# Optimization experiments

Measured on AMD Instinct MI355X. Metric: run time of the kernel, lower is better.

Reference implementation:

```python
import jax, jax.numpy as jnp
import numpy as np

H = 16      # q heads
G = 4       # groups (n_rep)
THETA = 10000.0


def _rope(x, cos, sin):
    # x pairs adjacent elements (torch complex view of reshape(..., -1, 2))
    x0 = x[..., ::2]
    x1 = x[..., 1::2]
    r0 = x0 * cos - x1 * sin
    r1 = x0 * sin + x1 * cos
    return jnp.stack([r0, r1], axis=-1).reshape(x.shape)


def setup_inputs() -> dict:
    key = jax.random.key(0)
    ks = jax.random.split(key, 5)
    B, S, D = 2, 2048, 1024
    return {
        "x": jax.random.normal(ks[0], (B, S, D), jnp.float32),
        "Wq": jax.random.normal(ks[1], (D, D), jnp.float32) * 0.02,
        "Wk": jax.random.normal(ks[2], (D, D // G), jnp.float32) * 0.02,
        "Wv": jax.random.normal(ks[3], (D, D // G), jnp.float32) * 0.02,
        "Wo": jax.random.normal(ks[4], (D, D), jnp.float32) * 0.02,
    }


def reference(x, Wq, Wk, Wv, Wo):
    B, S, D = x.shape
    hd = D // H                     # head dim = 64
    Hkv = H // G                    # kv heads = 4

    q = x @ Wq                      # (B,S,D)
    k = x @ Wk                      # (B,S,D/G)
    v = x @ Wv                      # (B,S,D/G)

    # repeat_kv: (B,S,Hkv,hd) -> (B,S,H,hd)
    k = jnp.repeat(k.reshape(B, S, Hkv, hd), G, axis=2)
    v = jnp.repeat(v.reshape(B, S, Hkv, hd), G, axis=2)

    # RoPE angles: freqs precomputed over hidden_dim (as in source)
    inv = 1.0 / (THETA ** (jnp.arange(0, D, 2, dtype=jnp.float32) / D))  # (D/2,)
    ang = jnp.arange(S, dtype=jnp.float32)[:, None] * inv[None, :]       # (S,D/2)
    q = _rope(q, jnp.cos(ang)[None], jnp.sin(ang)[None])                 # (B,S,D)
    angk = ang[:, : hd // 2]                                             # (S,hd/2)
    k = _rope(k, jnp.cos(angk)[None, :, None, :], jnp.sin(angk)[None, :, None, :])

    q = q.reshape(B, S, H, hd).transpose(0, 2, 1, 3)   # (B,H,S,hd)
    k = k.transpose(0, 2, 1, 3)
    v = v.transpose(0, 2, 1, 3)

    # NOTE: scale uses sqrt(hidden_dim), faithful to source
    scores = jnp.einsum('bhqd,bhkd->bhqk', q, k) / jnp.sqrt(jnp.float32(D))
    p = jax.nn.softmax(scores, axis=-1)
    o = jnp.einsum('bhqk,bhkd->bhqd', p, v)
    o = o.transpose(0, 2, 1, 3).reshape(B, S, D)
    return o @ Wo
```

## Files before the change

### kernel.cpp

```cpp
#include <hip/hip_runtime.h>
#include <math.h>

#define BATCH 2
#define SEQ   2048
#define DMODEL 1024
#define KDIM  1024
#define NH    16
#define HDIM  64
#define GRP   4
#define NKV   4
#define NSPLIT 4

enum { M_PLAIN = 0, M_QKV = 1 };

#define LN_THETA 9.210340371976184f

typedef short bf8_t __attribute__((ext_vector_type(8)));
typedef float f4_t __attribute__((ext_vector_type(4)));
typedef unsigned short us4_t __attribute__((ext_vector_type(4)));
typedef unsigned short us8_t __attribute__((ext_vector_type(8)));
typedef _Float16 h_t;
typedef _Float16 h4_t __attribute__((ext_vector_type(4)));

#define QB_OFF 0
#define KB_OFF 4194304
#define VB_OFF (4194304 + 1048576)

__device__ __forceinline__ unsigned short f2bf(float f) {
  unsigned int u = __float_as_uint(f);
  u += 0x7fffu + ((u >> 16) & 1u);
  return (unsigned short)(u >> 16);
}

__device__ __forceinline__ void gload_lds16(const void* g, void* l) {
  typedef __attribute__((address_space(1))) unsigned int gu32;
  typedef __attribute__((address_space(3))) unsigned int lu32;
  __builtin_amdgcn_global_load_lds((const gu32*)g, (lu32*)l, 16, 0, 0);
}

__global__ __launch_bounds__(256) void conv_x(const float* __restrict__ in,
                                              unsigned short* __restrict__ out) {
  const int i = blockIdx.x * 256 + threadIdx.x;
  float4 v = ((const float4*)in)[i];
  us4_t o = {f2bf(v.x), f2bf(v.y), f2bf(v.z), f2bf(v.w)};
  ((us4_t*)out)[i] = o;
}

__global__ __launch_bounds__(256) void convT_all(const float* __restrict__ W0,
                                                 const float* __restrict__ W1,
                                                 const float* __restrict__ W2,
                                                 const float* __restrict__ W3,
                                                 unsigned short* __restrict__ Wqkvt,
                                                 unsigned short* __restrict__ Wot) {
  const float* W; unsigned short* out; int N, rowoff;
  switch (blockIdx.z) {
    case 0: W = W0; out = Wqkvt; N = 1024; rowoff = 0;    break;
    case 1: W = W1; out = Wqkvt; N = 256;  rowoff = 1024; break;
    case 2: W = W2; out = Wqkvt; N = 256;  rowoff = 1280; break;
    default: W = W3; out = Wot;  N = 1024; rowoff = 0;    break;
  }
  const int n0 = blockIdx.x * 64;
  if (n0 >= N) return;
  __shared__ unsigned short T[64][72];
  const int t = threadIdx.x;
  const int k0 = blockIdx.y * 64;
  const int kr = t >> 4, n4 = (t & 15) * 4;
#pragma unroll
  for (int i = 0; i < 4; ++i) {
    const int k = kr + i * 16;
    float4 v = *(const float4*)&W[(size_t)(k0 + k) * N + n0 + n4];
    T[n4 + 0][k] = f2bf(v.x);
    T[n4 + 1][k] = f2bf(v.y);
    T[n4 + 2][k] = f2bf(v.z);
    T[n4 + 3][k] = f2bf(v.w);
  }
  __syncthreads();
#pragma unroll
  for (int i = 0; i < 2; ++i) {
    const int c = t + i * 256;
    const int n = c >> 3, kc = (c & 7) * 8;
    us8_t v = *(const us8_t*)&T[n][kc];
    *(us8_t*)&out[(size_t)(rowoff + n0 + n) * KDIM + k0 + kc] = v;
  }
}

template <int MODE>
__global__ __launch_bounds__(256, 3) void gemm_bf16(const unsigned short* __restrict__ A,
                                                    const unsigned short* __restrict__ Bt,
                                                    void* __restrict__ Cdst_, int N) {
  __shared__ __align__(16) unsigned short As[64 * 64];
  __shared__ __align__(16) unsigned short Bs[128 * 64];

  const int tid = threadIdx.x;
  const int lane = tid & 63, quad = lane >> 4, l16 = lane & 15;
  const int w = tid >> 6, wm = w >> 1, wn = w & 1;
  const int row0 = blockIdx.x * 64, col0 = blockIdx.y * 128;

  const int m0 = tid >> 2;
  const int kc0 = (tid & 3) ^ ((m0 >> 1) & 3);
  const unsigned short* Ag0 = A + (size_t)(row0 + m0) * KDIM + kc0 * 8;
  const unsigned short* Bg0 = Bt + (size_t)(col0 + m0) * KDIM + kc0 * 8;
  unsigned short* Al0 = &As[tid * 8];
  unsigned short* Bl0 = &Bs[tid * 8];

  int aoff[2][2], boff[4][2];
#pragma unroll
  for (int mi = 0; mi < 2; ++mi) {
    const int am = wm * 32 + mi * 16 + l16;
    const int sw = quad ^ ((am >> 1) & 3);
#pragma unroll
    for (int kh = 0; kh < 2; ++kh)
      aoff[mi][kh] = kh * 2048 + (((am << 2) | sw) << 3);
  }
#pragma unroll
  for (int ni = 0; ni < 4; ++ni) {
    const int bn = wn * 64 + ni * 16 + l16;
    const int sw = quad ^ ((bn >> 1) & 3);
#pragma unroll
    for (int kh = 0; kh < 2; ++kh)
      boff[ni][kh] = kh * 4096 + (((bn << 2) | sw) << 3);
  }

  f4_t acc[2][4];
#pragma unroll
  for (int mi = 0; mi < 2; ++mi)
#pragma unroll
    for (int ni = 0; ni < 4; ++ni) acc[mi][ni] = (f4_t){0.f, 0.f, 0.f, 0.f};

  for (int kb = 0; kb < KDIM; kb += 64) {
    __syncthreads();
    gload_lds16(Ag0 + kb,       Al0);
    gload_lds16(Ag0 + kb + 32,  Al0 + 2048);
    gload_lds16(Bg0 + kb,                     Bl0);
    gload_lds16(Bg0 + (size_t)64 * KDIM + kb, Bl0 + 2048);
    gload_lds16(Bg0 + kb + 32,                     Bl0 + 4096);
    gload_lds16(Bg0 + (size_t)64 * KDIM + kb + 32, Bl0 + 6144);
    __syncthreads();

    bf8_t af[2][2], bfr[4][2];
#pragma unroll
    for (int mi = 0; mi < 2; ++mi)
#pragma unroll
      for (int kh = 0; kh < 2; ++kh) af[mi][kh] = *(const bf8_t*)&As[aoff[mi][kh]];
#pragma unroll
    for (int ni = 0; ni < 4; ++ni)
#pragma unroll
      for (int kh = 0; kh < 2; ++kh) bfr[ni][kh] = *(const bf8_t*)&Bs[boff[ni][kh]];
#pragma unroll
    for (int kh = 0; kh < 2; ++kh)
#pragma unroll
      for (int mi = 0; mi < 2; ++mi)
#pragma unroll
        for (int ni = 0; ni < 4; ++ni)
          acc[mi][ni] = __builtin_amdgcn_mfma_f32_16x16x32_bf16(af[mi][kh], bfr[ni][kh], acc[mi][ni], 0, 0, 0);
  }

  if constexpr (MODE == M_PLAIN) {
    float* out = (float*)Cdst_;
#pragma unroll
    for (int mi = 0; mi < 2; ++mi) {
      const int rowb = row0 + wm * 32 + mi * 16 + quad * 4;
#pragma unroll
      for (int ni = 0; ni < 4; ++ni) {
        const int n = col0 + wn * 64 + ni * 16 + l16;
#pragma unroll
        for (int r = 0; r < 4; ++r)
          out[(size_t)(rowb + r) * N + n] = acc[mi][ni][r];
      }
    }
  } else {
    unsigned short* Qb = (unsigned short*)Cdst_;
    unsigned short* Kb = Qb + (KB_OFF - QB_OFF);
    unsigned short* Vb = Qb + (VB_OFF - QB_OFF);
#pragma unroll
    for (int ni = 0; ni < 4; ++ni) {
      const int nb = col0 + wn * 64 + ni * 16;
      const int n = nb + l16;
      if (nb < 1024) {
        const float inv = expf(-(float)(2 * (n >> 1)) * (LN_THETA / (float)DMODEL));
        const float sgn = (n & 1) ? 1.f : -1.f;
        const int h = n >> 6, d = n & 63;
#pragma unroll
        for (int mi = 0; mi < 2; ++mi) {
          const int rowb = row0 + wm * 32 + mi * 16 + quad * 4;
#pragma unroll
          for (int r = 0; r < 4; ++r) {
            const int row = rowb + r;
            const int bb = row >> 11, s = row & (SEQ - 1);
            const float v = acc[mi][ni][r];
            const float p = __shfl_xor(v, 1);
            float sn, cs;
            sincosf((float)s * inv, &sn, &cs);
            const float res = (v * cs + sgn * p * sn) * 0.03125f;
            Qb[((size_t)(bb * NH + h) * SEQ + s) * HDIM + d] = f2bf(res);
          }
        }
      } else if (nb < 1280) {
        const int nk = n - 1024;
        const int hkv = nk >> 6, d = nk & 63;
        const float inv = expf(-(float)(2 * (d >> 1)) * (LN_THETA / (float)DMODEL));
        const float sgn = (nk & 1) ? 1.f : -1.f;
#pragma unroll
        for (int mi = 0; mi < 2; ++mi) {
          const int rowb = row0 + wm * 32 + mi * 16 + quad * 4;
#pragma unroll
          for (int r = 0; r < 4; ++r) {
            const int row = rowb + r;
            const int bb = row >> 11, s = row & (SEQ - 1);
            const float v = acc[mi][ni][r];
            const float p = __shfl_xor(v, 1);
            float sn, cs;
            sincosf((float)s * inv, &sn, &cs);
            const float res = v * cs + sgn * p * sn;
            Kb[((size_t)(bb * NKV + hkv) * SEQ + s) * HDIM + d] = f2bf(res);
          }
        }
      } else {
        const int nv = n - 1280;
        const int hkv = nv >> 6, d = nv & 63;
#pragma unroll
        for (int mi = 0; mi < 2; ++mi) {
          const int s0 = row0 + wm * 32 + mi * 16 + quad * 4;
          const int bb = s0 >> 11, sl = s0 & (SEQ - 1);
          const int st = sl & 63;
          const int ps = (sl & ~63) | (st & 0x20) | ((st & 0x0C) << 1) | ((st & 0x10) >> 2);
          us4_t stv = {f2bf(acc[mi][ni][0]), f2bf(acc[mi][ni][1]),
                       f2bf(acc[mi][ni][2]), f2bf(acc[mi][ni][3])};
          *(us4_t*)&Vb[((size_t)(bb * NKV + hkv) * HDIM + d) * SEQ + ps] = stv;
        }
      }
    }
  }
}

__global__ __launch_bounds__(256, 4) void attn_fwd(const unsigned short* __restrict__ Q,
                                                   const unsigned short* __restrict__ K,
                                                   const unsigned short* __restrict__ V,
                                                   h_t* __restrict__ Opart,
                                                   float* __restrict__ Lpart) {
  __shared__ __align__(16) unsigned short Kt[4096];
  __shared__ __align__(16) unsigned short Vt[4096];

  const int b = blockIdx.x >> 4;
  const int h = blockIdx.x & (NH - 1);
  const int hkv = h >> 2;
  const int q0 = blockIdx.y * 128;
  const int sp = blockIdx.z;
  const int tid = threadIdx.x;
  const int w = tid >> 6;
  const int lane = tid & 63;
  const int quad = lane >> 4;
  const int l16 = lane & 15;

  const unsigned short* Qg = Q + ((size_t)(b * NH + h) * SEQ + q0 + w * 32) * HDIM;
  const unsigned short* Kg = K + (size_t)(b * NKV + hkv) * SEQ * HDIM;
  const unsigned short* Vg = V + (size_t)(b * NKV + hkv) * HDIM * SEQ;

  bf8_t qb[2][2];
#pragma unroll
  for (int g = 0; g < 2; ++g)
#pragma unroll
    for (int half = 0; half < 2; ++half)
      qb[g][half] = *(const bf8_t*)(Qg + (size_t)(g * 16 + l16) * HDIM + half * 32 + quad * 8);

  f4_t accO[2][4];
#pragma unroll
  for (int g = 0; g < 2; ++g)
#pragma unroll
    for (int d = 0; d < 4; ++d) accO[g][d] = (f4_t){0.f, 0.f, 0.f, 0.f};
  float accLs[2] = {0.f, 0.f};

  const int sw8 = (quad ^ ((l16 >> 1) & 3)) << 3;

  const int skey = tid >> 2;
  const int gc = ((tid & 3) ^ ((tid >> 3) & 3)) << 3;
  const unsigned short* KgA = Kg + (size_t)skey * HDIM + gc;
  const unsigned short* VgA = Vg + (size_t)skey * SEQ + gc;

  const int kbeg = sp * (SEQ / NSPLIT);
  const int kend = kbeg + SEQ / NSPLIT;
  for (int k0 = kbeg; k0 < kend; k0 += 64) {
    __syncthreads();
    gload_lds16(KgA + (size_t)k0 * HDIM,      &Kt[tid * 8]);
    gload_lds16(KgA + (size_t)k0 * HDIM + 32, &Kt[tid * 8 + 2048]);
    gload_lds16(VgA + k0,      &Vt[tid * 8]);
    gload_lds16(VgA + k0 + 32, &Vt[tid * 8 + 2048]);
    __syncthreads();

    union { bf8_t bf; unsigned int dw[4]; } pa[2][2];
#pragma unroll
    for (int cb = 0; cb < 4; ++cb) {
      const int koff = (cb * 16 + l16) * 32 + sw8;
      bf8_t kf0 = *(const bf8_t*)&Kt[koff];
      bf8_t kf1 = *(const bf8_t*)&Kt[koff + 2048];
#pragma unroll
      for (int g = 0; g < 2; ++g) {
        f4_t s = (f4_t){0.f, 0.f, 0.f, 0.f};
        s = __builtin_amdgcn_mfma_f32_16x16x32_bf16(kf0, qb[g][0], s, 0, 0, 0);
        s = __builtin_amdgcn_mfma_f32_16x16x32_bf16(kf1, qb[g][1], s, 0, 0, 0);
        const float p0 = __expf(s[0]), p1 = __expf(s[1]);
        const float p2 = __expf(s[2]), p3 = __expf(s[3]);
        accLs[g] += (p0 + p1) + (p2 + p3);
        pa[g][cb >> 1].dw[(cb & 1) * 2 + 0] =
            __builtin_amdgcn_perm(__float_as_uint(p1) + 0x8000u,
                                  __float_as_uint(p0) + 0x8000u, 0x07060302u);
        pa[g][cb >> 1].dw[(cb & 1) * 2 + 1] =
            __builtin_amdgcn_perm(__float_as_uint(p3) + 0x8000u,
                                  __float_as_uint(p2) + 0x8000u, 0x07060302u);
      }
    }

#pragma unroll
    for (int db = 0; db < 4; ++db) {
      const int voff = (db * 16 + l16) * 32 + sw8;
      bf8_t vf0 = *(const bf8_t*)&Vt[voff];
      bf8_t vf1 = *(const bf8_t*)&Vt[voff + 2048];
#pragma unroll
      for (int g = 0; g < 2; ++g) {
        accO[g][db] = __builtin_amdgcn_mfma_f32_16x16x32_bf16(pa[g][0].bf, vf0, accO[g][db], 0, 0, 0);
        accO[g][db] = __builtin_amdgcn_mfma_f32_16x16x32_bf16(pa[g][1].bf, vf1, accO[g][db], 0, 0, 0);
      }
    }
  }

#pragma unroll
  for (int g = 0; g < 2; ++g) {
    accLs[g] += __shfl_xor(accLs[g], 16);
    accLs[g] += __shfl_xor(accLs[g], 32);
  }

  h_t* Osp = Opart + (size_t)sp * BATCH * SEQ * NH * HDIM;
  float* Lsp = Lpart + (size_t)sp * BATCH * SEQ * NH;
#pragma unroll
  for (int g = 0; g < 2; ++g)
#pragma unroll
    for (int r = 0; r < 4; ++r) {
      const int q = q0 + w * 32 + g * 16 + quad * 4 + r;
      const size_t rowi = ((size_t)b * SEQ + q) * NH + h;
      h_t* op = Osp + rowi * HDIM;
#pragma unroll
      for (int db = 0; db < 4; ++db)
        op[db * 16 + l16] = (h_t)accO[g][db][r];
    }
  if (quad == 0) {
#pragma unroll
    for (int g = 0; g < 2; ++g) {
      const int q = q0 + w * 32 + g * 16 + l16;
      Lsp[((size_t)b * SEQ + q) * NH + h] = accLs[g];
    }
  }
}

__global__ __launch_bounds__(256) void attn_merge(const h_t* __restrict__ Opart,
                                                  const float* __restrict__ Lpart,
                                                  unsigned short* __restrict__ Ow) {
  const int idx = blockIdx.x * 256 + threadIdx.x;
  const int g = idx >> 4, j = (idx & 15) * 4;
  const size_t nq = (size_t)BATCH * SEQ * NH;
  float L = 0.f;
  float4 acc = make_float4(0.f, 0.f, 0.f, 0.f);
#pragma unroll
  for (int u = 0; u < NSPLIT; ++u) {
    L += Lpart[u * nq + g];
    h4_t o = *(const h4_t*)&Opart[((size_t)u * nq + g) * HDIM + j];
    acc.x += (float)o[0]; acc.y += (float)o[1];
    acc.z += (float)o[2]; acc.w += (float)o[3];
  }
  const float il = 1.0f / L;
  us4_t o = {f2bf(acc.x * il), f2bf(acc.y * il), f2bf(acc.z * il), f2bf(acc.w * il)};
  *(us4_t*)&Ow[(size_t)g * HDIM + j] = o;
}

extern "C" void kernel_launch(void* const* d_in, const int* in_sizes, int n_in,
                              void* d_out, int out_size, void* d_ws, size_t ws_size,
                              hipStream_t stream) {
  (void)in_sizes; (void)n_in; (void)out_size; (void)ws_size;
  const float* x  = (const float*)d_in[0];
  const float* Wq = (const float*)d_in[1];
  const float* Wk = (const float*)d_in[2];
  const float* Wv = (const float*)d_in[3];
  const float* Wo = (const float*)d_in[4];
  float* out = (float*)d_out;

  unsigned short* Qb    = (unsigned short*)d_ws;
  unsigned short* Kb    = Qb + 4194304;
  unsigned short* Vb    = Kb + 1048576;
  unsigned short* xb    = Vb + 1048576;
  unsigned short* Owb   = xb + 4194304;
  unsigned short* Wqkvt = Owb + 4194304;
  unsigned short* Wot   = Wqkvt + 1572864;
  h_t* Opart = (h_t*)(Wot + 1048576);
  float* Lpart = (float*)(Opart + (size_t)NSPLIT * 4194304);

  dim3 blk(256);
  conv_x<<<dim3(4096), blk, 0, stream>>>(x, xb);
  convT_all<<<dim3(16, 16, 4), blk, 0, stream>>>(Wq, Wk, Wv, Wo, Wqkvt, Wot);

  gemm_bf16<M_QKV><<<dim3(64, 12), blk, 0, stream>>>(xb, Wqkvt, Qb, 1536);
  attn_fwd<<<dim3(BATCH * NH, SEQ / 128, NSPLIT), blk, 0, stream>>>(Qb, Kb, Vb, Opart, Lpart);
  attn_merge<<<dim3(4096), blk, 0, stream>>>(Opart, Lpart, Owb);
  gemm_bf16<M_PLAIN><<<dim3(64, 8), blk, 0, stream>>>(Owb, Wot, out, DMODEL);
}
```

Measured before the change: 172.3 us.

## Double-buffer K/V tiles in attention and fold log2e into Q scale

Adds a second LDS buffer for the K and V tiles so the global-to-LDS copy of the next 64-key tile is issued before computing on the current one. This leaves one barrier per iteration instead of two and lets the copy overlap the MFMA and exp work. The Q pre-scale now includes log2(e), so the softmax uses exp2f directly and drops one multiply per score. LDS use per block doubles, which may cut the number of resident blocks.

```diff
diff --git a/kernel.cpp b/kernel.cpp
--- a/kernel.cpp
+++ b/kernel.cpp
@@ -14,6 +14,7 @@
 enum { M_PLAIN = 0, M_QKV = 1 };
 
 #define LN_THETA 9.210340371976184f
+#define QSCALE 0.0450842200965f
 
 typedef short bf8_t __attribute__((ext_vector_type(8)));
 typedef float f4_t __attribute__((ext_vector_type(4)));
@@ -191,7 +192,7 @@
             const float p = __shfl_xor(v, 1);
             float sn, cs;
             sincosf((float)s * inv, &sn, &cs);
-            const float res = (v * cs + sgn * p * sn) * 0.03125f;
+            const float res = (v * cs + sgn * p * sn) * QSCALE;
             Qb[((size_t)(bb * NH + h) * SEQ + s) * HDIM + d] = f2bf(res);
           }
         }
@@ -238,8 +239,8 @@
                                                    const unsigned short* __restrict__ V,
                                                    h_t* __restrict__ Opart,
                                                    float* __restrict__ Lpart) {
-  __shared__ __align__(16) unsigned short Kt[4096];
-  __shared__ __align__(16) unsigned short Vt[4096];
+  __shared__ __align__(16) unsigned short Kt[2][4096];
+  __shared__ __align__(16) unsigned short Vt[2][4096];
 
   const int b = blockIdx.x >> 4;
   const int h = blockIdx.x & (NH - 1);
@@ -278,28 +279,39 @@
   const unsigned short* VgA = Vg + (size_t)skey * SEQ + gc;
 
   const int kbeg = sp * (SEQ / NSPLIT);
-  const int kend = kbeg + SEQ / NSPLIT;
-  for (int k0 = kbeg; k0 < kend; k0 += 64) {
+  const int NT = (SEQ / NSPLIT) / 64;
+
+  gload_lds16(KgA + (size_t)kbeg * HDIM,      &Kt[0][tid * 8]);
+  gload_lds16(KgA + (size_t)kbeg * HDIM + 32, &Kt[0][tid * 8 + 2048]);
+  gload_lds16(VgA + kbeg,      &Vt[0][tid * 8]);
+  gload_lds16(VgA + kbeg + 32, &Vt[0][tid * 8 + 2048]);
+
+  for (int t = 0; t < NT; ++t) {
+    const int cur = t & 1;
     __syncthreads();
-    gload_lds16(KgA + (size_t)k0 * HDIM,      &Kt[tid * 8]);
-    gload_lds16(KgA + (size_t)k0 * HDIM + 32, &Kt[tid * 8 + 2048]);
-    gload_lds16(VgA + k0,      &Vt[tid * 8]);
-    gload_lds16(VgA + k0 + 32, &Vt[tid * 8 + 2048]);
-    __syncthreads();
+    if (t + 1 < NT) {
+      const int kn = kbeg + (t + 1) * 64;
+      gload_lds16(KgA + (size_t)kn * HDIM,      &Kt[1 - cur][tid * 8]);
+      gload_lds16(KgA + (size_t)kn * HDIM + 32, &Kt[1 - cur][tid * 8 + 2048]);
+      gload_lds16(VgA + kn,      &Vt[1 - cur][tid * 8]);
+      gload_lds16(VgA + kn + 32, &Vt[1 - cur][tid * 8 + 2048]);
+    }
+    const unsigned short* Ktc = Kt[cur];
+    const unsigned short* Vtc = Vt[cur];
 
     union { bf8_t bf; unsigned int dw[4]; } pa[2][2];
 #pragma unroll
     for (int cb = 0; cb < 4; ++cb) {
       const int koff = (cb * 16 + l16) * 32 + sw8;
-      bf8_t kf0 = *(const bf8_t*)&Kt[koff];
-      bf8_t kf1 = *(const bf8_t*)&Kt[koff + 2048];
+      bf8_t kf0 = *(const bf8_t*)&Ktc[koff];
+      bf8_t kf1 = *(const bf8_t*)&Ktc[koff + 2048];
 #pragma unroll
       for (int g = 0; g < 2; ++g) {
         f4_t s = (f4_t){0.f, 0.f, 0.f, 0.f};
         s = __builtin_amdgcn_mfma_f32_16x16x32_bf16(kf0, qb[g][0], s, 0, 0, 0);
         s = __builtin_amdgcn_mfma_f32_16x16x32_bf16(kf1, qb[g][1], s, 0, 0, 0);
-        const float p0 = __expf(s[0]), p1 = __expf(s[1]);
-        const float p2 = __expf(s[2]), p3 = __expf(s[3]);
+        const float p0 = exp2f(s[0]), p1 = exp2f(s[1]);
+        const float p2 = exp2f(s[2]), p3 = exp2f(s[3]);
         accLs[g] += (p0 + p1) + (p2 + p3);
         pa[g][cb >> 1].dw[(cb & 1) * 2 + 0] =
             __builtin_amdgcn_perm(__float_as_uint(p1) + 0x8000u,
@@ -313,8 +325,8 @@
 #pragma unroll
     for (int db = 0; db < 4; ++db) {
       const int voff = (db * 16 + l16) * 32 + sw8;
-      bf8_t vf0 = *(const bf8_t*)&Vt[voff];
-      bf8_t vf1 = *(const bf8_t*)&Vt[voff + 2048];
+      bf8_t vf0 = *(const bf8_t*)&Vtc[voff];
+      bf8_t vf1 = *(const bf8_t*)&Vtc[voff + 2048];
 #pragma unroll
       for (int g = 0; g < 2; ++g) {
         accO[g][db] = __builtin_amdgcn_mfma_f32_16x16x32_bf16(pa[g][0].bf, vf0, accO[g][db], 0, 0, 0);
```

Result: slower. 180.5 us (+4.8%).

## Double attention query tile per block, interleave QK/PV halves, fold log2e into Q

Applied to the files above, without the earlier changes.

Each warp now processes 64 query rows instead of 32, so each K/V tile loaded into LDS is reused across twice as many queries and the grid shrinks by half. The key tile is processed in two 32-key halves, with PV MMAs issued right after each half's probabilities, which shortens P register lifetime. The Q pre-scale now folds in log2(e) so the softmax can use exp2f instead of __expf. The costs are higher register pressure (launch bounds drop from 4 to 3 waves) and fewer blocks to spread across CUs.

```diff
diff --git a/kernel.cpp b/kernel.cpp
--- a/kernel.cpp
+++ b/kernel.cpp
@@ -14,6 +14,7 @@
 enum { M_PLAIN = 0, M_QKV = 1 };
 
 #define LN_THETA 9.210340371976184f
+#define QSCALE 0.0450842200965f
 
 typedef short bf8_t __attribute__((ext_vector_type(8)));
 typedef float f4_t __attribute__((ext_vector_type(4)));
@@ -191,7 +192,7 @@
             const float p = __shfl_xor(v, 1);
             float sn, cs;
             sincosf((float)s * inv, &sn, &cs);
-            const float res = (v * cs + sgn * p * sn) * 0.03125f;
+            const float res = (v * cs + sgn * p * sn) * QSCALE;
             Qb[((size_t)(bb * NH + h) * SEQ + s) * HDIM + d] = f2bf(res);
           }
         }
@@ -233,7 +234,7 @@
   }
 }
 
-__global__ __launch_bounds__(256, 4) void attn_fwd(const unsigned short* __restrict__ Q,
+__global__ __launch_bounds__(256, 3) void attn_fwd(const unsigned short* __restrict__ Q,
                                                    const unsigned short* __restrict__ K,
                                                    const unsigned short* __restrict__ V,
                                                    h_t* __restrict__ Opart,
@@ -244,7 +245,7 @@
   const int b = blockIdx.x >> 4;
   const int h = blockIdx.x & (NH - 1);
   const int hkv = h >> 2;
-  const int q0 = blockIdx.y * 128;
+  const int q0 = blockIdx.y * 256;
   const int sp = blockIdx.z;
   const int tid = threadIdx.x;
   const int w = tid >> 6;
@@ -252,23 +253,23 @@
   const int quad = lane >> 4;
   const int l16 = lane & 15;
 
-  const unsigned short* Qg = Q + ((size_t)(b * NH + h) * SEQ + q0 + w * 32) * HDIM;
+  const unsigned short* Qg = Q + ((size_t)(b * NH + h) * SEQ + q0 + w * 64) * HDIM;
   const unsigned short* Kg = K + (size_t)(b * NKV + hkv) * SEQ * HDIM;
   const unsigned short* Vg = V + (size_t)(b * NKV + hkv) * HDIM * SEQ;
 
-  bf8_t qb[2][2];
-#pragma unroll
-  for (int g = 0; g < 2; ++g)
+  bf8_t qb[4][2];
+#pragma unroll
+  for (int g = 0; g < 4; ++g)
 #pragma unroll
     for (int half = 0; half < 2; ++half)
       qb[g][half] = *(const bf8_t*)(Qg + (size_t)(g * 16 + l16) * HDIM + half * 32 + quad * 8);
 
-  f4_t accO[2][4];
-#pragma unroll
-  for (int g = 0; g < 2; ++g)
+  f4_t accO[4][4];
+#pragma unroll
+  for (int g = 0; g < 4; ++g)
 #pragma unroll
     for (int d = 0; d < 4; ++d) accO[g][d] = (f4_t){0.f, 0.f, 0.f, 0.f};
-  float accLs[2] = {0.f, 0.f};
+  float accLs[4] = {0.f, 0.f, 0.f, 0.f};
 
   const int sw8 = (quad ^ ((l16 >> 1) & 3)) << 3;
 
@@ -287,44 +288,44 @@
     gload_lds16(VgA + k0 + 32, &Vt[tid * 8 + 2048]);
     __syncthreads();
 
-    union { bf8_t bf; unsigned int dw[4]; } pa[2][2];
-#pragma unroll
-    for (int cb = 0; cb < 4; ++cb) {
-      const int koff = (cb * 16 + l16) * 32 + sw8;
-      bf8_t kf0 = *(const bf8_t*)&Kt[koff];
-      bf8_t kf1 = *(const bf8_t*)&Kt[koff + 2048];
-#pragma unroll
-      for (int g = 0; g < 2; ++g) {
-        f4_t s = (f4_t){0.f, 0.f, 0.f, 0.f};
-        s = __builtin_amdgcn_mfma_f32_16x16x32_bf16(kf0, qb[g][0], s, 0, 0, 0);
-        s = __builtin_amdgcn_mfma_f32_16x16x32_bf16(kf1, qb[g][1], s, 0, 0, 0);
-        const float p0 = __expf(s[0]), p1 = __expf(s[1]);
-        const float p2 = __expf(s[2]), p3 = __expf(s[3]);
-        accLs[g] += (p0 + p1) + (p2 + p3);
-        pa[g][cb >> 1].dw[(cb & 1) * 2 + 0] =
-            __builtin_amdgcn_perm(__float_as_uint(p1) + 0x8000u,
-                                  __float_as_uint(p0) + 0x8000u, 0x07060302u);
-        pa[g][cb >> 1].dw[(cb & 1) * 2 + 1] =
-            __builtin_amdgcn_perm(__float_as_uint(p3) + 0x8000u,
-                                  __float_as_uint(p2) + 0x8000u, 0x07060302u);
+#pragma unroll
+    for (int kh = 0; kh < 2; ++kh) {
+      union { bf8_t bf; unsigned int dw[4]; } pa[4];
+#pragma unroll
+      for (int cbh = 0; cbh < 2; ++cbh) {
+        const int cb = kh * 2 + cbh;
+        const int koff = (cb * 16 + l16) * 32 + sw8;
+        bf8_t kf0 = *(const bf8_t*)&Kt[koff];
+        bf8_t kf1 = *(const bf8_t*)&Kt[koff + 2048];
+#pragma unroll
+        for (int g = 0; g < 4; ++g) {
+          f4_t s = (f4_t){0.f, 0.f, 0.f, 0.f};
+          s = __builtin_amdgcn_mfma_f32_16x16x32_bf16(kf0, qb[g][0], s, 0, 0, 0);
+          s = __builtin_amdgcn_mfma_f32_16x16x32_bf16(kf1, qb[g][1], s, 0, 0, 0);
+          const float p0 = exp2f(s[0]), p1 = exp2f(s[1]);
+          const float p2 = exp2f(s[2]), p3 = exp2f(s[3]);
+          accLs[g] += (p0 + p1) + (p2 + p3);
+          pa[g].dw[cbh * 2 + 0] =
+              __builtin_amdgcn_perm(__float_as_uint(p1) + 0x8000u,
+                                    __float_as_uint(p0) + 0x8000u, 0x07060302u);
+          pa[g].dw[cbh * 2 + 1] =
+              __builtin_amdgcn_perm(__float_as_uint(p3) + 0x8000u,
+                                    __float_as_uint(p2) + 0x8000u, 0x07060302u);
+        }
+      }
+#pragma unroll
+      for (int db = 0; db < 4; ++db) {
+        const int voff = (db * 16 + l16) * 32 + sw8 + kh * 2048;
+        bf8_t vf = *(const bf8_t*)&Vt[voff];
+#pragma unroll
+        for (int g = 0; g < 4; ++g)
+          accO[g][db] = __builtin_amdgcn_mfma_f32_16x16x32_bf16(pa[g].bf, vf, accO[g][db], 0, 0, 0);
       }
     }
-
-#pragma unroll
-    for (int db = 0; db < 4; ++db) {
-      const int voff = (db * 16 + l16) * 32 + sw8;
-      bf8_t vf0 = *(const bf8_t*)&Vt[voff];
-      bf8_t vf1 = *(const bf8_t*)&Vt[voff + 2048];
-#pragma unroll
-      for (int g = 0; g < 2; ++g) {
-        accO[g][db] = __builtin_amdgcn_mfma_f32_16x16x32_bf16(pa[g][0].bf, vf0, accO[g][db], 0, 0, 0);
-        accO[g][db] = __builtin_amdgcn_mfma_f32_16x16x32_bf16(pa[g][1].bf, vf1, accO[g][db], 0, 0, 0);
-      }
-    }
-  }
-
-#pragma unroll
-  for (int g = 0; g < 2; ++g) {
+  }
+
+#pragma unroll
+  for (int g = 0; g < 4; ++g) {
     accLs[g] += __shfl_xor(accLs[g], 16);
     accLs[g] += __shfl_xor(accLs[g], 32);
   }
@@ -332,10 +333,10 @@
   h_t* Osp = Opart + (size_t)sp * BATCH * SEQ * NH * HDIM;
   float* Lsp = Lpart + (size_t)sp * BATCH * SEQ * NH;
 #pragma unroll
-  for (int g = 0; g < 2; ++g)
+  for (int g = 0; g < 4; ++g)
 #pragma unroll
     for (int r = 0; r < 4; ++r) {
-      const int q = q0 + w * 32 + g * 16 + quad * 4 + r;
+      const int q = q0 + w * 64 + g * 16 + quad * 4 + r;
       const size_t rowi = ((size_t)b * SEQ + q) * NH + h;
       h_t* op = Osp + rowi * HDIM;
 #pragma unroll
@@ -344,8 +345,8 @@
     }
   if (quad == 0) {
 #pragma unroll
-    for (int g = 0; g < 2; ++g) {
-      const int q = q0 + w * 32 + g * 16 + l16;
+    for (int g = 0; g < 4; ++g) {
+      const int q = q0 + w * 64 + g * 16 + l16;
       Lsp[((size_t)b * SEQ + q) * NH + h] = accLs[g];
     }
   }
@@ -397,7 +398,7 @@
   convT_all<<<dim3(16, 16, 4), blk, 0, stream>>>(Wq, Wk, Wv, Wo, Wqkvt, Wot);
 
   gemm_bf16<M_QKV><<<dim3(64, 12), blk, 0, stream>>>(xb, Wqkvt, Qb, 1536);
-  attn_fwd<<<dim3(BATCH * NH, SEQ / 128, NSPLIT), blk, 0, stream>>>(Qb, Kb, Vb, Opart, Lpart);
+  attn_fwd<<<dim3(BATCH * NH, SEQ / 256, NSPLIT), blk, 0, stream>>>(Qb, Kb, Vb, Opart, Lpart);
   attn_merge<<<dim3(4096), blk, 0, stream>>>(Opart, Lpart, Owb);
   gemm_bf16<M_PLAIN><<<dim3(64, 8), blk, 0, stream>>>(Owb, Wot, out, DMODEL);
 }
```

After: 232.1 us. 34.7% more time.
